# Optimization experiments

Hardware: AMD Instinct MI355X
Metric: run time of the kernel (lower is better)

Reference implementation:

```python
import jax, jax.numpy as jnp
import numpy as np

E, TOPK = 8, 2
N_EMBD, TEXT_DIM, FULL = 1024, 1024, 1024
BS, SEQ = 8, 512

def setup_inputs() -> dict:
    key = jax.random.key(0)
    ks = jax.random.split(key, 8)
    return {
        "x": jax.random.normal(ks[0], (BS, SEQ, N_EMBD), jnp.float32),
        "dec_embeddings": jax.random.normal(ks[1], (BS, TEXT_DIM), jnp.float32),
        # router is zero-init in the module, but use small random weights so top-k is non-degenerate
        "router_w": jax.random.normal(ks[2], (E, TEXT_DIM), jnp.float32) * 0.02,
        "router_b": jnp.zeros((E,), jnp.float32),
        "w1": jax.random.normal(ks[3], (E, N_EMBD, N_EMBD), jnp.float32) * 0.02,
        "w2": jax.random.normal(ks[4], (E, N_EMBD, FULL), jnp.float32) * 0.02,
        "b1": jnp.zeros((E, 1, N_EMBD), jnp.float32),
        "b2": jnp.zeros((E, 1, FULL), jnp.float32),
    }

def reference(x, dec_embeddings, router_w, router_b, w1, w2, b1, b2):
    bs, seqlen, n_embd = x.shape
    logits = dec_embeddings @ router_w.T + router_b          # (bs, E)
    gate_probs = jax.nn.softmax(logits, axis=-1)
    topk_w, topk_idx = jax.lax.top_k(gate_probs, TOPK)       # (bs, k)
    topk_w = topk_w / jnp.sum(topk_w, axis=-1, keepdims=True)
    # dense all-expert 2-layer MLP (as written in the original)
    hidden = jax.nn.relu(jnp.einsum('bsn,enh->ebsh', x, w1) + b1[:, None])   # (E,bs,S,H)
    out_all = jnp.einsum('ebsh,ehf->ebsf', hidden, w2) + b2[:, None]          # (E,bs,S,F)
    out_b = jnp.transpose(out_all, (1, 0, 2, 3))             # (bs,E,S,F)
    # gather top-k expert outputs per batch item and combine
    sel = jnp.take_along_axis(out_b, topk_idx[:, :, None, None], axis=1)      # (bs,k,S,F)
    final_output = jnp.sum(topk_w[:, :, None, None] * sel, axis=1)            # (bs,S,F)
    combined_mask = jnp.max(jax.nn.one_hot(topk_idx, E, dtype=x.dtype), axis=1)  # (bs,E)
    aux_loss = E * jnp.sum(jnp.mean(gate_probs, axis=0) * jnp.mean(combined_mask, axis=0))
    return final_output, aux_loss, combined_mask, logits
```

## Files before the change

### kernel.cpp

```cpp
#include <hip/hip_runtime.h>
#include <hip/hip_bf16.h>
#include <stdint.h>

#define EXP 8
#define DIM 1024
#define SEQL 512
#define BATCH 8
#define OUT_FINAL_N (BATCH * SEQL * DIM)
#define OFF_AUX    4194304
#define OFF_MASK   4194305
#define OFF_LOGITS 4194369

typedef __bf16 bf16_t;
typedef bf16_t bf16x8 __attribute__((ext_vector_type(8)));
typedef bf16_t bf16x4 __attribute__((ext_vector_type(4)));
typedef float  f32x4  __attribute__((ext_vector_type(4)));

typedef __attribute__((address_space(1))) void* as1p;
typedef __attribute__((address_space(3))) void* as3p;

__device__ __forceinline__ void glds16(const void* g, void* l) {
  __builtin_amdgcn_global_load_lds((as1p)(void*)g, (as3p)l, 16, 0, 0);
}

__global__ void router_kernel(const float* __restrict__ dec,
                              const float* __restrict__ rw,
                              const float* __restrict__ rb,
                              float* __restrict__ out_aux,
                              float* __restrict__ out_mask,
                              float* __restrict__ out_logits,
                              int* __restrict__ idx_ws,
                              float* __restrict__ w_ws) {
  __shared__ float part[256];
  __shared__ float lg[64];
  __shared__ float probs[64];
  __shared__ float msk[64];
  const int tid = threadIdx.x;
  const int p = tid >> 2, seg = tid & 3;
  const int b = p >> 3, e = p & 7;
  const float4* dv = (const float4*)(dec + b * DIM + seg * 256);
  const float4* wv = (const float4*)(rw + e * DIM + seg * 256);
  float s = 0.f;
#pragma unroll 8
  for (int i = 0; i < 64; ++i) {
    float4 a = dv[i], c = wv[i];
    s += a.x * c.x + a.y * c.y + a.z * c.z + a.w * c.w;
  }
  part[tid] = s;
  __syncthreads();
  if (seg == 0) {
    float l = part[tid] + part[tid + 1] + part[tid + 2] + part[tid + 3] + rb[e];
    lg[p] = l;
    out_logits[p] = l;
  }
  __syncthreads();
  if (tid < 8) {
    float l[8];
    float mx = -1e30f;
#pragma unroll
    for (int k = 0; k < 8; ++k) { l[k] = lg[tid * 8 + k]; mx = fmaxf(mx, l[k]); }
    float pe[8];
    float sum = 0.f;
#pragma unroll
    for (int k = 0; k < 8; ++k) { pe[k] = expf(l[k] - mx); sum += pe[k]; }
    float inv = 1.f / sum;
#pragma unroll
    for (int k = 0; k < 8; ++k) { pe[k] *= inv; probs[tid * 8 + k] = pe[k]; }
    int i0 = 0;
#pragma unroll
    for (int k = 1; k < 8; ++k) if (pe[k] > pe[i0]) i0 = k;
    int i1 = (i0 == 0) ? 1 : 0;
#pragma unroll
    for (int k = 0; k < 8; ++k) if (k != i0 && pe[k] > pe[i1]) i1 = k;
    float p0 = pe[i0], p1 = pe[i1];
    float invs = 1.f / (p0 + p1);
    idx_ws[tid * 2] = i0;
    idx_ws[tid * 2 + 1] = i1;
    w_ws[tid * 2] = p0 * invs;
    w_ws[tid * 2 + 1] = p1 * invs;
#pragma unroll
    for (int k = 0; k < 8; ++k) {
      float m = (k == i0 || k == i1) ? 1.f : 0.f;
      msk[tid * 8 + k] = m;
      out_mask[tid * 8 + k] = m;
    }
  }
  __syncthreads();
  if (tid == 0) {
    float aux = 0.f;
#pragma unroll
    for (int k = 0; k < 8; ++k) {
      float mp = 0.f, mm = 0.f;
#pragma unroll
      for (int bb = 0; bb < 8; ++bb) { mp += probs[bb * 8 + k]; mm += msk[bb * 8 + k]; }
      aux += (mp * 0.125f) * (mm * 0.125f);
    }
    out_aux[0] = 8.f * aux;
  }
}

__global__ void cast_x_kernel(const float* __restrict__ x, bf16_t* __restrict__ xb) {
  const int i = blockIdx.x * 256 + threadIdx.x;
  float4 v = ((const float4*)x)[i];
  bf16x4 o;
  o[0] = (bf16_t)v.x; o[1] = (bf16_t)v.y; o[2] = (bf16_t)v.z; o[3] = (bf16_t)v.w;
  ((bf16x4*)xb)[i] = o;
}

__global__ void transpose_cast_kernel(const float* __restrict__ w1,
                                      const float* __restrict__ w2,
                                      bf16_t* __restrict__ w1t,
                                      bf16_t* __restrict__ w2t) {
  __shared__ float tile[32][33];
  const int z = blockIdx.z;
  const float* src = (z < 8) ? (w1 + (size_t)z * DIM * DIM) : (w2 + (size_t)(z - 8) * DIM * DIM);
  bf16_t* dst = (z < 8) ? (w1t + (size_t)z * DIM * DIM) : (w2t + (size_t)(z - 8) * DIM * DIM);
  const int tx = threadIdx.x, ty = threadIdx.y;
  const int c0 = blockIdx.x * 32, r0 = blockIdx.y * 32;
#pragma unroll
  for (int j = 0; j < 32; j += 8) tile[ty + j][tx] = src[(size_t)(r0 + ty + j) * DIM + c0 + tx];
  __syncthreads();
#pragma unroll
  for (int j = 0; j < 32; j += 8)
    dst[(size_t)(c0 + ty + j) * DIM + r0 + tx] = (bf16_t)tile[tx][ty + j];
}

__device__ __forceinline__ void gemm_kloop(const bf16_t* __restrict__ A,
                                           const bf16_t* __restrict__ Bt,
                                           char* sA, char* sB,
                                           int tid, f32x4 acc[4][4]) {
  const int lane = tid & 63;
  const int w = tid >> 6;
  const int wr = w >> 1, wc = w & 1;
  const int m15 = lane & 15, q = lane >> 4;

  const int rl = tid >> 2;
  const int cp = (tid & 3) ^ (rl & 3);
  const bf16_t* ga0 = A + (size_t)rl * DIM + cp * 8;
  const bf16_t* ga1 = ga0 + (size_t)64 * DIM;
  const bf16_t* gb0 = Bt + (size_t)rl * DIM + cp * 8;
  const bf16_t* gb1 = gb0 + (size_t)64 * DIM;
  char* la0 = sA + tid * 16;
  char* la1 = sA + 4096 + tid * 16;
  char* lb0 = sB + tid * 16;
  char* lb1 = sB + 4096 + tid * 16;

  const char* ra[4];
  const char* rb[4];
#pragma unroll
  for (int i = 0; i < 4; ++i) {
    int r = wr * 64 + i * 16 + m15;
    ra[i] = sA + r * 64 + ((q ^ (r & 3)) * 16);
    int n = wc * 64 + i * 16 + m15;
    rb[i] = sB + n * 64 + ((q ^ (n & 3)) * 16);
  }

  for (int kt = 0; kt < DIM; kt += 32) {
    glds16(ga0 + kt, la0);
    glds16(ga1 + kt, la1);
    glds16(gb0 + kt, lb0);
    glds16(gb1 + kt, lb1);
    __syncthreads();
    bf16x8 af[4], bfr[4];
#pragma unroll
    for (int i = 0; i < 4; ++i) af[i] = *(const bf16x8*)ra[i];
#pragma unroll
    for (int j = 0; j < 4; ++j) bfr[j] = *(const bf16x8*)rb[j];
#pragma unroll
    for (int i = 0; i < 4; ++i)
#pragma unroll
      for (int j = 0; j < 4; ++j)
        acc[i][j] = __builtin_amdgcn_mfma_f32_16x16x32_bf16(af[i], bfr[j], acc[i][j], 0, 0, 0);
    __syncthreads();
  }
}

__global__ __launch_bounds__(256) void gemm1_kernel(const bf16_t* __restrict__ xb,
                                                    const bf16_t* __restrict__ w1t,
                                                    const float* __restrict__ b1,
                                                    const int* __restrict__ topk_idx,
                                                    bf16_t* __restrict__ hidden) {
  __shared__ __align__(16) char smem[16384];
  const int tid = threadIdx.x;
  const int bN = blockIdx.x, bM = blockIdx.y, slot = blockIdx.z;
  const int b = slot >> 1;
  const int e = topk_idx[slot];

  const bf16_t* A = xb + ((size_t)b * SEQL + bM * 128) * DIM;
  const bf16_t* Bt = w1t + ((size_t)e * DIM + bN * 128) * DIM;

  f32x4 acc[4][4];
#pragma unroll
  for (int i = 0; i < 4; ++i)
#pragma unroll
    for (int j = 0; j < 4; ++j) acc[i][j] = {0.f, 0.f, 0.f, 0.f};

  gemm_kloop(A, Bt, smem, smem + 8192, tid, acc);

  const int lane = tid & 63, w = tid >> 6;
  const int wr = w >> 1, wc = w & 1;
  const int m15 = lane & 15, q = lane >> 4;
  const float* be = b1 + e * DIM;
  bf16_t* H = hidden + (size_t)slot * SEQL * DIM;
#pragma unroll
  for (int i = 0; i < 4; ++i) {
    int row = bM * 128 + wr * 64 + i * 16 + q * 4;
#pragma unroll
    for (int j = 0; j < 4; ++j) {
      int col = bN * 128 + wc * 64 + j * 16 + m15;
      float bias = be[col];
#pragma unroll
      for (int r = 0; r < 4; ++r) {
        float v = acc[i][j][r] + bias;
        H[(size_t)(row + r) * DIM + col] = (bf16_t)fmaxf(v, 0.f);
      }
    }
  }
}

__global__ __launch_bounds__(256) void gemm2_kernel(const bf16_t* __restrict__ hidden,
                                                    const bf16_t* __restrict__ w2t,
                                                    const float* __restrict__ b2,
                                                    const int* __restrict__ topk_idx,
                                                    const float* __restrict__ topk_w,
                                                    float* __restrict__ out) {
  __shared__ __align__(16) char smem[16384];
  const int tid = threadIdx.x;
  const int bN = blockIdx.x, bM = blockIdx.y, b = blockIdx.z;
  const int e0 = topk_idx[b * 2], e1 = topk_idx[b * 2 + 1];
  const float w0 = topk_w[b * 2], w1v = topk_w[b * 2 + 1];

  f32x4 acc[4][4];
#pragma unroll
  for (int i = 0; i < 4; ++i)
#pragma unroll
    for (int j = 0; j < 4; ++j) acc[i][j] = {0.f, 0.f, 0.f, 0.f};

  const bf16_t* A0 = hidden + ((size_t)(b * 2) * SEQL + bM * 128) * DIM;
  const bf16_t* B0 = w2t + ((size_t)e0 * DIM + bN * 128) * DIM;
  gemm_kloop(A0, B0, smem, smem + 8192, tid, acc);

  const float s = w0 / w1v;
#pragma unroll
  for (int i = 0; i < 4; ++i)
#pragma unroll
    for (int j = 0; j < 4; ++j) acc[i][j] *= s;

  const bf16_t* A1 = hidden + ((size_t)(b * 2 + 1) * SEQL + bM * 128) * DIM;
  const bf16_t* B1 = w2t + ((size_t)e1 * DIM + bN * 128) * DIM;
  gemm_kloop(A1, B1, smem, smem + 8192, tid, acc);

  const int lane = tid & 63, w = tid >> 6;
  const int wr = w >> 1, wc = w & 1;
  const int m15 = lane & 15, q = lane >> 4;
  const float* be0 = b2 + e0 * DIM;
  const float* be1 = b2 + e1 * DIM;
  float* O = out + (size_t)b * SEQL * DIM;
#pragma unroll
  for (int i = 0; i < 4; ++i) {
    int row = bM * 128 + wr * 64 + i * 16 + q * 4;
#pragma unroll
    for (int j = 0; j < 4; ++j) {
      int col = bN * 128 + wc * 64 + j * 16 + m15;
      float bb = w0 * be0[col] + w1v * be1[col];
#pragma unroll
      for (int r = 0; r < 4; ++r) {
        O[(size_t)(row + r) * DIM + col] = w1v * acc[i][j][r] + bb;
      }
    }
  }
}

extern "C" void kernel_launch(void* const* d_in, const int* in_sizes, int n_in,
                              void* d_out, int out_size, void* d_ws, size_t ws_size,
                              hipStream_t stream) {
  const float* x   = (const float*)d_in[0];
  const float* dec = (const float*)d_in[1];
  const float* rw  = (const float*)d_in[2];
  const float* rb  = (const float*)d_in[3];
  const float* w1  = (const float*)d_in[4];
  const float* w2  = (const float*)d_in[5];
  const float* b1  = (const float*)d_in[6];
  const float* b2  = (const float*)d_in[7];
  float* out = (float*)d_out;

  char* ws = (char*)d_ws;
  bf16_t* xb   = (bf16_t*)(ws);
  bf16_t* w1t  = (bf16_t*)(ws + (8u << 20));
  bf16_t* w2t  = (bf16_t*)(ws + (24u << 20));
  bf16_t* hid  = (bf16_t*)(ws + (40u << 20));
  int*    idxw = (int*)(ws + (56u << 20));
  float*  ww   = (float*)(ws + (56u << 20) + 64);

  hipLaunchKernelGGL(router_kernel, dim3(1), dim3(256), 0, stream,
                     dec, rw, rb, out + OFF_AUX, out + OFF_MASK, out + OFF_LOGITS, idxw, ww);
  hipLaunchKernelGGL(cast_x_kernel, dim3(4096), dim3(256), 0, stream, x, xb);
  hipLaunchKernelGGL(transpose_cast_kernel, dim3(32, 32, 16), dim3(32, 8), 0, stream,
                     w1, w2, w1t, w2t);
  hipLaunchKernelGGL(gemm1_kernel, dim3(8, 4, 16), dim3(256), 0, stream,
                     xb, w1t, b1, idxw, hid);
  hipLaunchKernelGGL(gemm2_kernel, dim3(8, 4, 8), dim3(256), 0, stream,
                     hid, w2t, b2, idxw, ww, out);
}
```

Before: 221.6 us.

## Fuse prep kernels into one launch and split gemm2 experts across warp groups

The router, x-cast and weight transpose-cast kernels become one prep kernel that dispatches on block index. The transpose now uses 64x64 tiles with float4 loads and bf16x4 stores. gemm2 goes from 256 to 512 threads: each half of the block computes one expert's GEMM at the same time instead of running the two in sequence, and the two results are combined through shared memory. This halves gemm2's serial K-loop length per block at the cost of more registers and LDS per block, which may lower occupancy. The prep kernel also carries a 64x65 float tile, so the router block takes on LDS it does not need.

```diff
diff --git a/kernel.cpp b/kernel.cpp
--- a/kernel.cpp
+++ b/kernel.cpp
@@ -23,106 +23,123 @@
   __builtin_amdgcn_global_load_lds((as1p)(void*)g, (as3p)l, 16, 0, 0);
 }
 
-__global__ void router_kernel(const float* __restrict__ dec,
-                              const float* __restrict__ rw,
-                              const float* __restrict__ rb,
-                              float* __restrict__ out_aux,
-                              float* __restrict__ out_mask,
-                              float* __restrict__ out_logits,
-                              int* __restrict__ idx_ws,
-                              float* __restrict__ w_ws) {
+__global__ __launch_bounds__(256) void prep_kernel(
+    const float* __restrict__ x, const float* __restrict__ dec,
+    const float* __restrict__ rw, const float* __restrict__ rb,
+    const float* __restrict__ w1, const float* __restrict__ w2,
+    bf16_t* __restrict__ xb, bf16_t* __restrict__ w1t, bf16_t* __restrict__ w2t,
+    float* __restrict__ out_aux, float* __restrict__ out_mask,
+    float* __restrict__ out_logits, int* __restrict__ idx_ws,
+    float* __restrict__ w_ws) {
+  __shared__ float tile[64][65];
   __shared__ float part[256];
-  __shared__ float lg[64];
+  __shared__ float lg64[64];
   __shared__ float probs[64];
   __shared__ float msk[64];
-  const int tid = threadIdx.x;
-  const int p = tid >> 2, seg = tid & 3;
-  const int b = p >> 3, e = p & 7;
-  const float4* dv = (const float4*)(dec + b * DIM + seg * 256);
-  const float4* wv = (const float4*)(rw + e * DIM + seg * 256);
-  float s = 0.f;
+  const int bid = blockIdx.x;
+  const int t = threadIdx.x;
+
+  if (bid < 4096) {
+    const int z = bid >> 8;
+    const int rem = bid & 255;
+    const int r0 = (rem >> 4) * 64, c0 = (rem & 15) * 64;
+    const float* src = (z < 8) ? (w1 + (size_t)z * DIM * DIM)
+                               : (w2 + (size_t)(z - 8) * DIM * DIM);
+    bf16_t* dst = (z < 8) ? (w1t + (size_t)z * DIM * DIM)
+                          : (w2t + (size_t)(z - 8) * DIM * DIM);
+    const int rr = t >> 4, cc = t & 15;
+#pragma unroll
+    for (int i = 0; i < 4; ++i) {
+      const int row = rr + i * 16;
+      const float4 v = *(const float4*)(src + (size_t)(r0 + row) * DIM + c0 + cc * 4);
+      tile[row][cc * 4 + 0] = v.x;
+      tile[row][cc * 4 + 1] = v.y;
+      tile[row][cc * 4 + 2] = v.z;
+      tile[row][cc * 4 + 3] = v.w;
+    }
+    __syncthreads();
+#pragma unroll
+    for (int i = 0; i < 4; ++i) {
+      const int dc = rr + i * 16;
+      bf16x4 o;
+      o[0] = (bf16_t)tile[cc * 4 + 0][dc];
+      o[1] = (bf16_t)tile[cc * 4 + 1][dc];
+      o[2] = (bf16_t)tile[cc * 4 + 2][dc];
+      o[3] = (bf16_t)tile[cc * 4 + 3][dc];
+      *(bf16x4*)(dst + (size_t)(c0 + dc) * DIM + r0 + cc * 4) = o;
+    }
+  } else if (bid < 4096 + 1024) {
+    const int i0 = (bid - 4096) * 1024 + t;
+#pragma unroll
+    for (int i = 0; i < 4; ++i) {
+      float4 v = ((const float4*)x)[i0 + i * 256];
+      bf16x4 o;
+      o[0] = (bf16_t)v.x; o[1] = (bf16_t)v.y; o[2] = (bf16_t)v.z; o[3] = (bf16_t)v.w;
+      ((bf16x4*)xb)[i0 + i * 256] = o;
+    }
+  } else {
+    const int p = t >> 2, seg = t & 3;
+    const int b = p >> 3, e = p & 7;
+    const float4* dv = (const float4*)(dec + b * DIM + seg * 256);
+    const float4* wv = (const float4*)(rw + e * DIM + seg * 256);
+    float s = 0.f;
 #pragma unroll 8
-  for (int i = 0; i < 64; ++i) {
-    float4 a = dv[i], c = wv[i];
-    s += a.x * c.x + a.y * c.y + a.z * c.z + a.w * c.w;
-  }
-  part[tid] = s;
-  __syncthreads();
-  if (seg == 0) {
-    float l = part[tid] + part[tid + 1] + part[tid + 2] + part[tid + 3] + rb[e];
-    lg[p] = l;
-    out_logits[p] = l;
-  }
-  __syncthreads();
-  if (tid < 8) {
-    float l[8];
-    float mx = -1e30f;
-#pragma unroll
-    for (int k = 0; k < 8; ++k) { l[k] = lg[tid * 8 + k]; mx = fmaxf(mx, l[k]); }
-    float pe[8];
-    float sum = 0.f;
-#pragma unroll
-    for (int k = 0; k < 8; ++k) { pe[k] = expf(l[k] - mx); sum += pe[k]; }
-    float inv = 1.f / sum;
-#pragma unroll
-    for (int k = 0; k < 8; ++k) { pe[k] *= inv; probs[tid * 8 + k] = pe[k]; }
-    int i0 = 0;
-#pragma unroll
-    for (int k = 1; k < 8; ++k) if (pe[k] > pe[i0]) i0 = k;
-    int i1 = (i0 == 0) ? 1 : 0;
-#pragma unroll
-    for (int k = 0; k < 8; ++k) if (k != i0 && pe[k] > pe[i1]) i1 = k;
-    float p0 = pe[i0], p1 = pe[i1];
-    float invs = 1.f / (p0 + p1);
-    idx_ws[tid * 2] = i0;
-    idx_ws[tid * 2 + 1] = i1;
-    w_ws[tid * 2] = p0 * invs;
-    w_ws[tid * 2 + 1] = p1 * invs;
-#pragma unroll
-    for (int k = 0; k < 8; ++k) {
-      float m = (k == i0 || k == i1) ? 1.f : 0.f;
-      msk[tid * 8 + k] = m;
-      out_mask[tid * 8 + k] = m;
-    }
-  }
-  __syncthreads();
-  if (tid == 0) {
-    float aux = 0.f;
-#pragma unroll
-    for (int k = 0; k < 8; ++k) {
-      float mp = 0.f, mm = 0.f;
-#pragma unroll
-      for (int bb = 0; bb < 8; ++bb) { mp += probs[bb * 8 + k]; mm += msk[bb * 8 + k]; }
-      aux += (mp * 0.125f) * (mm * 0.125f);
-    }
-    out_aux[0] = 8.f * aux;
-  }
-}
-
-__global__ void cast_x_kernel(const float* __restrict__ x, bf16_t* __restrict__ xb) {
-  const int i = blockIdx.x * 256 + threadIdx.x;
-  float4 v = ((const float4*)x)[i];
-  bf16x4 o;
-  o[0] = (bf16_t)v.x; o[1] = (bf16_t)v.y; o[2] = (bf16_t)v.z; o[3] = (bf16_t)v.w;
-  ((bf16x4*)xb)[i] = o;
-}
-
-__global__ void transpose_cast_kernel(const float* __restrict__ w1,
-                                      const float* __restrict__ w2,
-                                      bf16_t* __restrict__ w1t,
-                                      bf16_t* __restrict__ w2t) {
-  __shared__ float tile[32][33];
-  const int z = blockIdx.z;
-  const float* src = (z < 8) ? (w1 + (size_t)z * DIM * DIM) : (w2 + (size_t)(z - 8) * DIM * DIM);
-  bf16_t* dst = (z < 8) ? (w1t + (size_t)z * DIM * DIM) : (w2t + (size_t)(z - 8) * DIM * DIM);
-  const int tx = threadIdx.x, ty = threadIdx.y;
-  const int c0 = blockIdx.x * 32, r0 = blockIdx.y * 32;
-#pragma unroll
-  for (int j = 0; j < 32; j += 8) tile[ty + j][tx] = src[(size_t)(r0 + ty + j) * DIM + c0 + tx];
-  __syncthreads();
-#pragma unroll
-  for (int j = 0; j < 32; j += 8)
-    dst[(size_t)(c0 + ty + j) * DIM + r0 + tx] = (bf16_t)tile[tx][ty + j];
+    for (int i = 0; i < 64; ++i) {
+      float4 a = dv[i], c = wv[i];
+      s += a.x * c.x + a.y * c.y + a.z * c.z + a.w * c.w;
+    }
+    part[t] = s;
+    __syncthreads();
+    if (seg == 0) {
+      float l = part[t] + part[t + 1] + part[t + 2] + part[t + 3] + rb[e];
+      lg64[p] = l;
+      out_logits[p] = l;
+    }
+    __syncthreads();
+    if (t < 8) {
+      float l[8];
+      float mx = -1e30f;
+#pragma unroll
+      for (int k = 0; k < 8; ++k) { l[k] = lg64[t * 8 + k]; mx = fmaxf(mx, l[k]); }
+      float pe[8];
+      float sum = 0.f;
+#pragma unroll
+      for (int k = 0; k < 8; ++k) { pe[k] = expf(l[k] - mx); sum += pe[k]; }
+      float inv = 1.f / sum;
+#pragma unroll
+      for (int k = 0; k < 8; ++k) { pe[k] *= inv; probs[t * 8 + k] = pe[k]; }
+      int i0 = 0;
+#pragma unroll
+      for (int k = 1; k < 8; ++k) if (pe[k] > pe[i0]) i0 = k;
+      int i1 = (i0 == 0) ? 1 : 0;
+#pragma unroll
+      for (int k = 0; k < 8; ++k) if (k != i0 && pe[k] > pe[i1]) i1 = k;
+      float p0 = pe[i0], p1 = pe[i1];
+      float invs = 1.f / (p0 + p1);
+      idx_ws[t * 2] = i0;
+      idx_ws[t * 2 + 1] = i1;
+      w_ws[t * 2] = p0 * invs;
+      w_ws[t * 2 + 1] = p1 * invs;
+#pragma unroll
+      for (int k = 0; k < 8; ++k) {
+        float m = (k == i0 || k == i1) ? 1.f : 0.f;
+        msk[t * 8 + k] = m;
+        out_mask[t * 8 + k] = m;
+      }
+    }
+    __syncthreads();
+    if (t == 0) {
+      float aux = 0.f;
+#pragma unroll
+      for (int k = 0; k < 8; ++k) {
+        float mp = 0.f, mm = 0.f;
+#pragma unroll
+        for (int bb = 0; bb < 8; ++bb) { mp += probs[bb * 8 + k]; mm += msk[bb * 8 + k]; }
+        aux += (mp * 0.125f) * (mm * 0.125f);
+      }
+      out_aux[0] = 8.f * aux;
+    }
+  }
 }
 
 __device__ __forceinline__ void gemm_kloop(const bf16_t* __restrict__ A,
@@ -218,54 +235,70 @@
   }
 }
 
-__global__ __launch_bounds__(256) void gemm2_kernel(const bf16_t* __restrict__ hidden,
+__global__ __launch_bounds__(512) void gemm2_kernel(const bf16_t* __restrict__ hidden,
                                                     const bf16_t* __restrict__ w2t,
                                                     const float* __restrict__ b2,
                                                     const int* __restrict__ topk_idx,
                                                     const float* __restrict__ topk_w,
                                                     float* __restrict__ out) {
-  __shared__ __align__(16) char smem[16384];
+  __shared__ __align__(16) char smem[32768];
   const int tid = threadIdx.x;
+  const int g = tid >> 8;
+  const int t = tid & 255;
   const int bN = blockIdx.x, bM = blockIdx.y, b = blockIdx.z;
-  const int e0 = topk_idx[b * 2], e1 = topk_idx[b * 2 + 1];
+  const int e = topk_idx[b * 2 + g];
+  const float sg = topk_w[b * 2 + g];
+
+  char* sA = smem + g * 16384;
+  char* sB = smem + g * 16384 + 8192;
+
+  f32x4 acc[4][4];
+#pragma unroll
+  for (int i = 0; i < 4; ++i)
+#pragma unroll
+    for (int j = 0; j < 4; ++j) acc[i][j] = {0.f, 0.f, 0.f, 0.f};
+
+  const bf16_t* A = hidden + ((size_t)(b * 2 + g) * SEQL + bM * 128) * DIM;
+  const bf16_t* Bt = w2t + ((size_t)e * DIM + bN * 128) * DIM;
+  gemm_kloop(A, Bt, sA, sB, t, acc);
+
+  float* scr = (float*)smem;
+  const int lane = t & 63, wv = t >> 6;
+  const int wr = wv >> 1, wc = wv & 1;
+  const int m15 = lane & 15, q = lane >> 4;
   const float w0 = topk_w[b * 2], w1v = topk_w[b * 2 + 1];
-
-  f32x4 acc[4][4];
-#pragma unroll
-  for (int i = 0; i < 4; ++i)
-#pragma unroll
-    for (int j = 0; j < 4; ++j) acc[i][j] = {0.f, 0.f, 0.f, 0.f};
-
-  const bf16_t* A0 = hidden + ((size_t)(b * 2) * SEQL + bM * 128) * DIM;
-  const bf16_t* B0 = w2t + ((size_t)e0 * DIM + bN * 128) * DIM;
-  gemm_kloop(A0, B0, smem, smem + 8192, tid, acc);
-
-  const float s = w0 / w1v;
-#pragma unroll
-  for (int i = 0; i < 4; ++i)
-#pragma unroll
-    for (int j = 0; j < 4; ++j) acc[i][j] *= s;
-
-  const bf16_t* A1 = hidden + ((size_t)(b * 2 + 1) * SEQL + bM * 128) * DIM;
-  const bf16_t* B1 = w2t + ((size_t)e1 * DIM + bN * 128) * DIM;
-  gemm_kloop(A1, B1, smem, smem + 8192, tid, acc);
-
-  const int lane = tid & 63, w = tid >> 6;
-  const int wr = w >> 1, wc = w & 1;
-  const int m15 = lane & 15, q = lane >> 4;
-  const float* be0 = b2 + e0 * DIM;
-  const float* be1 = b2 + e1 * DIM;
+  const float* be0 = b2 + topk_idx[b * 2] * DIM;
+  const float* be1 = b2 + topk_idx[b * 2 + 1] * DIM;
   float* O = out + (size_t)b * SEQL * DIM;
-#pragma unroll
-  for (int i = 0; i < 4; ++i) {
-    int row = bM * 128 + wr * 64 + i * 16 + q * 4;
-#pragma unroll
-    for (int j = 0; j < 4; ++j) {
-      int col = bN * 128 + wc * 64 + j * 16 + m15;
-      float bb = w0 * be0[col] + w1v * be1[col];
-#pragma unroll
-      for (int r = 0; r < 4; ++r) {
-        O[(size_t)(row + r) * DIM + col] = w1v * acc[i][j][r] + bb;
+
+#pragma unroll
+  for (int half = 0; half < 2; ++half) {
+    __syncthreads();
+    if (g == 1) {
+#pragma unroll
+      for (int ii = 0; ii < 2; ++ii)
+#pragma unroll
+        for (int j = 0; j < 4; ++j)
+#pragma unroll
+          for (int r = 0; r < 4; ++r)
+            scr[(ii * 16 + j * 4 + r) * 256 + t] = sg * acc[half * 2 + ii][j][r];
+    }
+    __syncthreads();
+    if (g == 0) {
+#pragma unroll
+      for (int ii = 0; ii < 2; ++ii) {
+        const int i = half * 2 + ii;
+        const int row = bM * 128 + wr * 64 + i * 16 + q * 4;
+#pragma unroll
+        for (int j = 0; j < 4; ++j) {
+          const int col = bN * 128 + wc * 64 + j * 16 + m15;
+          const float bb = w0 * be0[col] + w1v * be1[col];
+#pragma unroll
+          for (int r = 0; r < 4; ++r) {
+            O[(size_t)(row + r) * DIM + col] =
+                sg * acc[i][j][r] + scr[(ii * 16 + j * 4 + r) * 256 + t] + bb;
+          }
+        }
       }
     }
   }
@@ -292,13 +325,11 @@
   int*    idxw = (int*)(ws + (56u << 20));
   float*  ww   = (float*)(ws + (56u << 20) + 64);
 
-  hipLaunchKernelGGL(router_kernel, dim3(1), dim3(256), 0, stream,
-                     dec, rw, rb, out + OFF_AUX, out + OFF_MASK, out + OFF_LOGITS, idxw, ww);
-  hipLaunchKernelGGL(cast_x_kernel, dim3(4096), dim3(256), 0, stream, x, xb);
-  hipLaunchKernelGGL(transpose_cast_kernel, dim3(32, 32, 16), dim3(32, 8), 0, stream,
-                     w1, w2, w1t, w2t);
+  hipLaunchKernelGGL(prep_kernel, dim3(4096 + 1024 + 1), dim3(256), 0, stream,
+                     x, dec, rw, rb, w1, w2, xb, w1t, w2t,
+                     out + OFF_AUX, out + OFF_MASK, out + OFF_LOGITS, idxw, ww);
   hipLaunchKernelGGL(gemm1_kernel, dim3(8, 4, 16), dim3(256), 0, stream,
                      xb, w1t, b1, idxw, hid);
-  hipLaunchKernelGGL(gemm2_kernel, dim3(8, 4, 8), dim3(256), 0, stream,
+  hipLaunchKernelGGL(gemm2_kernel, dim3(8, 4, 8), dim3(512), 0, stream,
                      hid, w2t, b2, idxw, ww, out);
 }
```

Measured after the change: 206.9 us. 6.6% less time.
